# Optimization experiments

Measured on AMD Instinct MI355X. Metric: run time of the kernel, lower is better.

Reference implementation:

```python
import jax, jax.numpy as jnp
import numpy as np

ROI_SIZE = 5
BOX = 4.0  # hardcoded box_size in the module


def _bilinear(fm_b, y, x):
    """torchvision roi_align bilinear sample. fm_b: [C,H,W]; y,x: [N,P,P].
    Returns [N,C,P,P]."""
    C, H, W = fm_b.shape
    valid = (y > -1.0) & (y < H) & (x > -1.0) & (x < W)
    y = jnp.maximum(y, 0.0)
    x = jnp.maximum(x, 0.0)
    y0 = jnp.floor(y).astype(jnp.int32)
    x0 = jnp.floor(x).astype(jnp.int32)
    yc = y0 >= H - 1
    xc = x0 >= W - 1
    y0 = jnp.where(yc, H - 1, y0)
    x0 = jnp.where(xc, W - 1, x0)
    y1 = jnp.minimum(y0 + 1, H - 1)
    x1 = jnp.minimum(x0 + 1, W - 1)
    ly = jnp.where(yc, 0.0, y - y0)  # torchvision sets y=y_low at the top edge
    lx = jnp.where(xc, 0.0, x - x0)
    hy, hx = 1.0 - ly, 1.0 - lx
    # advanced indexing gathers -> [C,N,P,P]
    v00 = fm_b[:, y0, x0]
    v01 = fm_b[:, y0, x1]
    v10 = fm_b[:, y1, x0]
    v11 = fm_b[:, y1, x1]
    w00 = (hy * hx)[None]
    w01 = (hy * lx)[None]
    w10 = (ly * hx)[None]
    w11 = (ly * lx)[None]
    out = w00 * v00 + w01 * v01 + w10 * v10 + w11 * v11
    out = out * valid[None].astype(fm_b.dtype)
    return jnp.transpose(out, (1, 0, 2, 3))  # [N,C,P,P]


def _roi_align_points(fm_b, cand_b):
    """fm_b: [C,H,W]; cand_b: [N,2] (x,y). One sample per bin (sampling_ratio
    resolves to 1 since ceil(4/5)=1), spatial_scale=1, aligned=False."""
    bin_sz = BOX / ROI_SIZE
    off = (jnp.arange(ROI_SIZE, dtype=fm_b.dtype) + 0.5) * bin_sz  # bin centers
    xs = (cand_b[:, 0] - BOX / 2)[:, None] + off[None, :]  # [N,P]
    ys = (cand_b[:, 1] - BOX / 2)[:, None] + off[None, :]  # [N,P]
    Y = ys[:, :, None] * jnp.ones((1, 1, ROI_SIZE), fm_b.dtype)  # [N,P,P]
    X = xs[:, None, :] * jnp.ones((1, ROI_SIZE, 1), fm_b.dtype)
    Y = jnp.broadcast_to(ys[:, :, None], (ys.shape[0], ROI_SIZE, ROI_SIZE))
    X = jnp.broadcast_to(xs[:, None, :], (xs.shape[0], ROI_SIZE, ROI_SIZE))
    return _bilinear(fm_b, Y, X)  # [N,C,P,P]


def setup_inputs() -> dict:
    key = jax.random.key(0)
    k1, k2 = jax.random.split(key)
    B, C, H, W, N = 8, 256, 135, 240, 1024
    feature_map = jax.random.normal(k1, (B, C, H, W), dtype=jnp.float32)
    # (x, y) points in feature-map coordinates (spatial_scale=1.0)
    candidates = jax.random.uniform(k2, (B, N, 2), dtype=jnp.float32) * jnp.array(
        [W - 1.0, H - 1.0], dtype=jnp.float32
    )
    return {"feature_map": feature_map, "candidates": candidates}


def reference(feature_map, candidates):
    B, C, H, W = feature_map.shape
    N = candidates.shape[1]
    aligned = jax.vmap(_roi_align_points)(feature_map, candidates)  # [B,N,C,P,P]
    return aligned.reshape(B, N, C * ROI_SIZE * ROI_SIZE)
```

## Files before the change

### kernel.cpp

```cpp
#include <hip/hip_runtime.h>
#include <hip/hip_fp16.h>

#define ROI 5
#define NPTS 25
#define CCH 256
#define HH 135
#define WW 240
#define HWP (HH * WW)
#define NV4 (HWP / 4)
#define NB 8
#define NN 1024


struct Pt { int o00, o01, o10, o11; float w00, w01, w10, w11; int oo; };

__device__ __forceinline__ Pt prep(const float2* __restrict__ cb2, int idx) {
    Pt r;
    int n  = (idx * 5243) >> 17;
    int p  = idx - n * 25;
    int py = (p * 205) >> 10;
    int px = p - py * 5;

    float2 cc = cb2[n];

    float y = (cc.y - 2.0f) + ((float)py + 0.5f) * 0.8f;
    float x = (cc.x - 2.0f) + ((float)px + 0.5f) * 0.8f;
    bool valid = (y > -1.0f) && (y < (float)HH) && (x > -1.0f) && (x < (float)WW);
    y = fmaxf(y, 0.0f);
    x = fmaxf(x, 0.0f);
    int y0 = (int)y;
    int x0 = (int)x;
    bool yc = (y0 >= HH - 1);
    bool xc = (x0 >= WW - 1);
    if (yc) y0 = HH - 1;
    if (xc) x0 = WW - 1;
    int y1 = min(y0 + 1, HH - 1);
    int x1 = min(x0 + 1, WW - 1);
    float ly = yc ? 0.0f : y - (float)y0;
    float lx = xc ? 0.0f : x - (float)x0;
    float hy = 1.0f - ly, hx = 1.0f - lx;
    float vm = valid ? 1.0f : 0.0f;

    int r0 = y0 * WW, r1 = y1 * WW;
    r.o00 = r0 + x0; r.o01 = r0 + x1; r.o10 = r1 + x0; r.o11 = r1 + x1;
    float vhy = vm * hy, vly = vm * ly;
    r.w00 = vhy * hx; r.w01 = vhy * lx; r.w10 = vly * hx; r.w11 = vly * lx;
    r.oo = idx + n * 6375;
    return r;
}

__global__ __launch_bounds__(1024, 8) void roi_plane_ilp2(const float* __restrict__ fm,
                                                          const float* __restrict__ cand,
                                                          float* __restrict__ out) {
    __shared__ __half plane[HWP];

    int blk = blockIdx.x;
    int c   = blk & (CCH - 1);
    int b   = blk >> 8;
    int t   = threadIdx.x;

    const float4* src = (const float4*)(fm + ((size_t)b * CCH + c) * HWP);
    {
        float4 v0 = src[t];
        float4 v1 = src[1024 + t];
        float4 v2 = src[2048 + t];
        float4 v3 = src[3072 + t];
        __half2* d;
        d = (__half2*)(plane + (t) * 4);
        d[0] = __half2(__float2half(v0.x), __float2half(v0.y));
        d[1] = __half2(__float2half(v0.z), __float2half(v0.w));
        d = (__half2*)(plane + (1024 + t) * 4);
        d[0] = __half2(__float2half(v1.x), __float2half(v1.y));
        d[1] = __half2(__float2half(v1.z), __float2half(v1.w));
        d = (__half2*)(plane + (2048 + t) * 4);
        d[0] = __half2(__float2half(v2.x), __float2half(v2.y));
        d[1] = __half2(__float2half(v2.z), __float2half(v2.w));
        d = (__half2*)(plane + (3072 + t) * 4);
        d[0] = __half2(__float2half(v3.x), __float2half(v3.y));
        d[1] = __half2(__float2half(v3.z), __float2half(v3.w));

        float4 v4 = src[4096 + t];
        float4 v5 = src[5120 + t];
        float4 v6 = src[6144 + t];
        bool last = (t < NV4 - 7168);
        float4 v7 = last ? src[7168 + t] : make_float4(0.f, 0.f, 0.f, 0.f);
        d = (__half2*)(plane + (4096 + t) * 4);
        d[0] = __half2(__float2half(v4.x), __float2half(v4.y));
        d[1] = __half2(__float2half(v4.z), __float2half(v4.w));
        d = (__half2*)(plane + (5120 + t) * 4);
        d[0] = __half2(__float2half(v5.x), __float2half(v5.y));
        d[1] = __half2(__float2half(v5.z), __float2half(v5.w));
        d = (__half2*)(plane + (6144 + t) * 4);
        d[0] = __half2(__float2half(v6.x), __float2half(v6.y));
        d[1] = __half2(__float2half(v6.z), __float2half(v6.w));
        if (last) {
            d = (__half2*)(plane + (7168 + t) * 4);
            d[0] = __half2(__float2half(v7.x), __float2half(v7.y));
            d[1] = __half2(__float2half(v7.z), __float2half(v7.w));
        }
    }
    __syncthreads();

    const float2* cb2 = (const float2*)(cand + (size_t)b * NN * 2);
    float* obase = out + (size_t)b * NN * (CCH * NPTS) + c * NPTS;

#pragma unroll 1
    for (int k = 0; k < 12; k++) {
        int ia = k * 1024 + t;
        Pt A = prep(cb2, ia);
        Pt B = prep(cb2, ia + 12288);

        float a00 = __half2float(plane[A.o00]);
        float a01 = __half2float(plane[A.o01]);
        float a10 = __half2float(plane[A.o10]);
        float a11 = __half2float(plane[A.o11]);
        float b00 = __half2float(plane[B.o00]);
        float b01 = __half2float(plane[B.o01]);
        float b10 = __half2float(plane[B.o10]);
        float b11 = __half2float(plane[B.o11]);

        obase[A.oo] = A.w00 * a00 + A.w01 * a01 + A.w10 * a10 + A.w11 * a11;
        obase[B.oo] = B.w00 * b00 + B.w01 * b01 + B.w10 * b10 + B.w11 * b11;
    }
    {
        Pt A = prep(cb2, 24576 + t);
        float a00 = __half2float(plane[A.o00]);
        float a01 = __half2float(plane[A.o01]);
        float a10 = __half2float(plane[A.o10]);
        float a11 = __half2float(plane[A.o11]);
        obase[A.oo] = A.w00 * a00 + A.w01 * a01 + A.w10 * a10 + A.w11 * a11;
    }
}

extern "C" void kernel_launch(void* const* d_in, const int* in_sizes, int n_in,
                              void* d_out, int out_size, void* d_ws, size_t ws_size,
                              hipStream_t stream) {
    const float* fm   = (const float*)d_in[0];
    const float* cand = (const float*)d_in[1];
    float* out        = (float*)d_out;

    roi_plane_ilp2<<<NB * CCH, 1024, 0, stream>>>(fm, cand, out);
}
```

Before: 496.8 us.

## Map one candidate per thread with separable weights and vector stores

Reassigns work so each thread handles one candidate and all 25 sample points of the channel. It computes the row and column interpolation terms once per axis (5 each) instead of per point, and packs row/column byte offsets into 16-bit halves. Outputs are written as float4 groups. This cuts per-point index and weight arithmetic and store instruction count. In exchange each thread's 100-byte output run sits at a large stride from its neighbours', which weakens write coalescing, and the float4 stores are not 16-byte aligned for most channels.

```diff
diff --git a/kernel.cpp b/kernel.cpp
--- a/kernel.cpp
+++ b/kernel.cpp
@@ -1,7 +1,6 @@
 #include <hip/hip_runtime.h>
 #include <hip/hip_fp16.h>
 
-#define ROI 5
 #define NPTS 25
 #define CCH 256
 #define HH 135
@@ -11,47 +10,9 @@
 #define NB 8
 #define NN 1024
 
-
-struct Pt { int o00, o01, o10, o11; float w00, w01, w10, w11; int oo; };
-
-__device__ __forceinline__ Pt prep(const float2* __restrict__ cb2, int idx) {
-    Pt r;
-    int n  = (idx * 5243) >> 17;
-    int p  = idx - n * 25;
-    int py = (p * 205) >> 10;
-    int px = p - py * 5;
-
-    float2 cc = cb2[n];
-
-    float y = (cc.y - 2.0f) + ((float)py + 0.5f) * 0.8f;
-    float x = (cc.x - 2.0f) + ((float)px + 0.5f) * 0.8f;
-    bool valid = (y > -1.0f) && (y < (float)HH) && (x > -1.0f) && (x < (float)WW);
-    y = fmaxf(y, 0.0f);
-    x = fmaxf(x, 0.0f);
-    int y0 = (int)y;
-    int x0 = (int)x;
-    bool yc = (y0 >= HH - 1);
-    bool xc = (x0 >= WW - 1);
-    if (yc) y0 = HH - 1;
-    if (xc) x0 = WW - 1;
-    int y1 = min(y0 + 1, HH - 1);
-    int x1 = min(x0 + 1, WW - 1);
-    float ly = yc ? 0.0f : y - (float)y0;
-    float lx = xc ? 0.0f : x - (float)x0;
-    float hy = 1.0f - ly, hx = 1.0f - lx;
-    float vm = valid ? 1.0f : 0.0f;
-
-    int r0 = y0 * WW, r1 = y1 * WW;
-    r.o00 = r0 + x0; r.o01 = r0 + x1; r.o10 = r1 + x0; r.o11 = r1 + x1;
-    float vhy = vm * hy, vly = vm * ly;
-    r.w00 = vhy * hx; r.w01 = vhy * lx; r.w10 = vly * hx; r.w11 = vly * lx;
-    r.oo = idx + n * 6375;
-    return r;
-}
-
-__global__ __launch_bounds__(1024, 8) void roi_plane_ilp2(const float* __restrict__ fm,
-                                                          const float* __restrict__ cand,
-                                                          float* __restrict__ out) {
+__global__ __launch_bounds__(1024, 8) void roi_nmajor(const float* __restrict__ fm,
+                                                      const float* __restrict__ cand,
+                                                      float* __restrict__ out) {
     __shared__ __half plane[HWP];
 
     int blk = blockIdx.x;
@@ -99,36 +60,77 @@
             d[1] = __half2(__float2half(v7.z), __float2half(v7.w));
         }
     }
+
+    float2 cc = ((const float2*)cand)[(size_t)b * NN + t];
+    unsigned int ypk[5], xpk[5];
+    float Hy[5], Ly[5], Hx[5], Lx[5];
+#pragma unroll
+    for (int s = 0; s < 5; s++) {
+        float fs = ((float)s + 0.5f) * 0.8f;
+
+        float y = (cc.y - 2.0f) + fs;
+        float vy = ((y > -1.0f) && (y < (float)HH)) ? 1.0f : 0.0f;
+        y = fmaxf(y, 0.0f);
+        int y0 = (int)y;
+        bool ycl = (y0 >= HH - 1);
+        if (ycl) y0 = HH - 1;
+        int y1 = min(y0 + 1, HH - 1);
+        float ly = ycl ? 0.0f : y - (float)y0;
+        float hy = 1.0f - ly;
+        ypk[s] = (unsigned int)(y0 * (WW * 2)) | ((unsigned int)(y1 * (WW * 2)) << 16);
+        Hy[s] = vy * hy;
+        Ly[s] = vy * ly;
+
+        float x = (cc.x - 2.0f) + fs;
+        float vx = ((x > -1.0f) && (x < (float)WW)) ? 1.0f : 0.0f;
+        x = fmaxf(x, 0.0f);
+        int x0 = (int)x;
+        bool xcl = (x0 >= WW - 1);
+        if (xcl) x0 = WW - 1;
+        int x1 = min(x0 + 1, WW - 1);
+        float lx = xcl ? 0.0f : x - (float)x0;
+        float hx = 1.0f - lx;
+        xpk[s] = (unsigned int)(x0 * 2) | ((unsigned int)(x1 * 2) << 16);
+        Hx[s] = vx * hx;
+        Lx[s] = vx * lx;
+    }
     __syncthreads();
 
-    const float2* cb2 = (const float2*)(cand + (size_t)b * NN * 2);
-    float* obase = out + (size_t)b * NN * (CCH * NPTS) + c * NPTS;
+    const char* pl = (const char*)plane;
+    float* op = out + ((size_t)b * NN + t) * (CCH * NPTS) + c * NPTS;
 
-#pragma unroll 1
-    for (int k = 0; k < 12; k++) {
-        int ia = k * 1024 + t;
-        Pt A = prep(cb2, ia);
-        Pt B = prep(cb2, ia + 12288);
+    float q0 = 0.f, q1 = 0.f, q2 = 0.f;
+#pragma unroll
+    for (int k = 0; k < 24; k++) {
+        const int py = k / 5, px = k - (k / 5) * 5;
+        unsigned int yo = ypk[py], xo = xpk[px];
+        unsigned int ry0 = yo & 0xffffu, ry1 = yo >> 16;
+        unsigned int cx0 = xo & 0xffffu, cx1 = xo >> 16;
 
-        float a00 = __half2float(plane[A.o00]);
-        float a01 = __half2float(plane[A.o01]);
-        float a10 = __half2float(plane[A.o10]);
-        float a11 = __half2float(plane[A.o11]);
-        float b00 = __half2float(plane[B.o00]);
-        float b01 = __half2float(plane[B.o01]);
-        float b10 = __half2float(plane[B.o10]);
-        float b11 = __half2float(plane[B.o11]);
+        float v00 = __half2float(*(const __half*)(pl + (ry0 + cx0)));
+        float v01 = __half2float(*(const __half*)(pl + (ry0 + cx1)));
+        float v10 = __half2float(*(const __half*)(pl + (ry1 + cx0)));
+        float v11 = __half2float(*(const __half*)(pl + (ry1 + cx1)));
 
-        obase[A.oo] = A.w00 * a00 + A.w01 * a01 + A.w10 * a10 + A.w11 * a11;
-        obase[B.oo] = B.w00 * b00 + B.w01 * b01 + B.w10 * b10 + B.w11 * b11;
+        float r = (Hy[py] * Hx[px]) * v00 + (Hy[py] * Lx[px]) * v01
+                + (Ly[py] * Hx[px]) * v10 + (Ly[py] * Lx[px]) * v11;
+
+        const int m = k & 3;
+        if (m == 0)      q0 = r;
+        else if (m == 1) q1 = r;
+        else if (m == 2) q2 = r;
+        else *(float4*)(op + (k - 3)) = make_float4(q0, q1, q2, r);
     }
     {
-        Pt A = prep(cb2, 24576 + t);
-        float a00 = __half2float(plane[A.o00]);
-        float a01 = __half2float(plane[A.o01]);
-        float a10 = __half2float(plane[A.o10]);
-        float a11 = __half2float(plane[A.o11]);
-        obase[A.oo] = A.w00 * a00 + A.w01 * a01 + A.w10 * a10 + A.w11 * a11;
+        unsigned int yo = ypk[4], xo = xpk[4];
+        unsigned int ry0 = yo & 0xffffu, ry1 = yo >> 16;
+        unsigned int cx0 = xo & 0xffffu, cx1 = xo >> 16;
+        float v00 = __half2float(*(const __half*)(pl + (ry0 + cx0)));
+        float v01 = __half2float(*(const __half*)(pl + (ry0 + cx1)));
+        float v10 = __half2float(*(const __half*)(pl + (ry1 + cx0)));
+        float v11 = __half2float(*(const __half*)(pl + (ry1 + cx1)));
+        op[24] = (Hy[4] * Hx[4]) * v00 + (Hy[4] * Lx[4]) * v01
+               + (Ly[4] * Hx[4]) * v10 + (Ly[4] * Lx[4]) * v11;
     }
 }
 
@@ -139,5 +141,5 @@
     const float* cand = (const float*)d_in[1];
     float* out        = (float*)d_out;
 
-    roi_plane_ilp2<<<NB * CCH, 1024, 0, stream>>>(fm, cand, out);
+    roi_nmajor<<<NB * CCH, 1024, 0, stream>>>(fm, cand, out);
 }
```

After: 514.3 us. 1.04x slower.
